# Kernel tuning notes

Hardware: AMD Instinct MI355X
Metric: run time of the kernel (lower is better)

## Reference

```python
import jax, jax.numpy as jnp
import numpy as np

D_MODEL = 768
N_HEADS = 12
D_FF = 3072
EPS = 1e-6


def setup_inputs() -> dict:
    key = jax.random.key(0)
    ks = jax.random.split(key, 9)
    s = 0.02
    return {
        "x": jax.random.normal(ks[0], (2, 4096, D_MODEL), dtype=jnp.float32),
        "wq": jax.random.normal(ks[1], (D_MODEL, D_MODEL), dtype=jnp.float32) * s,
        "wk": jax.random.normal(ks[2], (D_MODEL, D_MODEL), dtype=jnp.float32) * s,
        "wv": jax.random.normal(ks[3], (D_MODEL, D_MODEL), dtype=jnp.float32) * s,
        "wo": jax.random.normal(ks[4], (D_MODEL, D_MODEL), dtype=jnp.float32) * s,
        "w1": jax.random.normal(ks[5], (D_MODEL, D_FF), dtype=jnp.float32) * s,
        "b1": jnp.zeros((D_FF,), dtype=jnp.float32),
        "w2": jax.random.normal(ks[6], (D_FF, D_MODEL), dtype=jnp.float32) * s,
        "b2": jnp.zeros((D_MODEL,), dtype=jnp.float32),
        "g1": jnp.ones((D_MODEL,), dtype=jnp.float32),
        "g2": jnp.ones((D_MODEL,), dtype=jnp.float32),
    }


def _rmsnorm(x, g):
    rms = jax.lax.rsqrt(jnp.mean(x * x, axis=-1, keepdims=True) + EPS)
    return x * rms * g


def _attn(x, wq, wk, wv, wo):
    B, T, D = x.shape
    H, Dh = N_HEADS, D // N_HEADS
    q = (x @ wq).reshape(B, T, H, Dh).transpose(0, 2, 1, 3)
    k = (x @ wk).reshape(B, T, H, Dh).transpose(0, 2, 1, 3)
    v = (x @ wv).reshape(B, T, H, Dh).transpose(0, 2, 1, 3)
    scores = jnp.einsum("bhqd,bhkd->bhqk", q, k) * (Dh ** -0.5)
    causal = jnp.triu(jnp.ones((T, T), dtype=bool), k=1)
    scores = jnp.where(causal, -jnp.inf, scores)
    attn = jax.nn.softmax(scores, axis=-1)
    out = jnp.einsum("bhqk,bhkd->bhqd", attn, v)
    out = out.transpose(0, 2, 1, 3).reshape(B, T, D)
    return out @ wo


def _ffn(x, w1, b1, w2, b2):
    h = jax.nn.gelu(x @ w1 + b1, approximate=False)
    return h @ w2 + b2


def reference(x, wq, wk, wv, wo, w1, b1, w2, b2, g1, g2):
    x = x + _attn(_rmsnorm(x, g1), wq, wk, wv, wo)
    x = x + _ffn(_rmsnorm(x, g2), w1, b1, w2, b2)
    return x
```

## Files before the change

kernel.cpp:

```cpp
#include <hip/hip_runtime.h>
#include <hip/hip_bf16.h>

typedef __attribute__((ext_vector_type(8))) short bf16x8;
typedef __attribute__((ext_vector_type(4))) short bf16x4;
typedef __attribute__((ext_vector_type(4))) float f32x4;

#define MFMA16(a, b, c) __builtin_amdgcn_mfma_f32_16x16x32_bf16((a), (b), (c), 0, 0, 0)

__device__ __forceinline__ f32x4 mfma_k16(bf16x4 a, bf16x4 b, f32x4 c) {
#if __has_builtin(__builtin_amdgcn_mfma_f32_16x16x16bf16_1k)
  return __builtin_amdgcn_mfma_f32_16x16x16bf16_1k(a, b, c, 0, 0, 0);
#elif __has_builtin(__builtin_amdgcn_mfma_f32_16x16x16_bf16)
  return __builtin_amdgcn_mfma_f32_16x16x16_bf16(a, b, c, 0, 0, 0);
#else
  asm("v_mfma_f32_16x16x16_bf16 %0, %1, %2, %0" : "+v"(c) : "v"(a), "v"(b));
  return c;
#endif
}

__device__ __forceinline__ ushort f2bf(float f) {
  union { __hip_bfloat16 h; ushort u; } cv;
  cv.h = __float2bfloat16(f);
  return cv.u;
}

__device__ __forceinline__ void gload16(const void* g, void* l) {
  __builtin_amdgcn_global_load_lds((const __attribute__((address_space(1))) void*)g,
                                   (__attribute__((address_space(3))) void*)l, 16, 0, 0);
}

__global__ void wtrans_all(const float* __restrict__ wq, const float* __restrict__ wk,
                           const float* __restrict__ wv, const float* __restrict__ wo,
                           const float* __restrict__ w1, const float* __restrict__ w2,
                           ushort* __restrict__ wqT, ushort* __restrict__ wkT,
                           ushort* __restrict__ wvT, ushort* __restrict__ woT,
                           ushort* __restrict__ w1T, ushort* __restrict__ w2T) {
  __shared__ float t[32][33];
  int id = blockIdx.x;
  const float* W;
  ushort* Wt;
  int K, N, nbx;
  if (id < 2304) {
    const int m = id / 576;
    id -= m * 576;
    W = (m == 0) ? wq : (m == 1) ? wk : (m == 2) ? wv : wo;
    Wt = (m == 0) ? wqT : (m == 1) ? wkT : (m == 2) ? wvT : woT;
    K = 768; N = 768; nbx = 24;
  } else if (id < 4608) {
    id -= 2304; W = w1; Wt = w1T; K = 768; N = 3072; nbx = 96;
  } else {
    id -= 4608; W = w2; Wt = w2T; K = 3072; N = 768; nbx = 24;
  }
  const int nb = (id % nbx) * 32, kb = (id / nbx) * 32;
  const int tx = threadIdx.x & 31, ty = threadIdx.x >> 5;
#pragma unroll
  for (int i = 0; i < 4; ++i)
    t[ty + i * 8][tx] = W[(size_t)(kb + ty + i * 8) * N + nb + tx];
  __syncthreads();
#pragma unroll
  for (int i = 0; i < 4; ++i)
    Wt[(size_t)(nb + ty + i * 8) * K + kb + tx] = f2bf(t[tx][ty + i * 8]);
}

__global__ void rmsnorm_kernel(const float* __restrict__ x, const float* __restrict__ g,
                               ushort* __restrict__ out) {
  const int row = blockIdx.x;
  const float* xr = x + (size_t)row * 768;
  const int t = threadIdx.x;
  float v0 = xr[t], v1 = xr[t + 256], v2 = xr[t + 512];
  float ss = v0 * v0 + v1 * v1 + v2 * v2;
#pragma unroll
  for (int off = 1; off < 64; off <<= 1) ss += __shfl_xor(ss, off);
  __shared__ float part[4];
  if ((t & 63) == 0) part[t >> 6] = ss;
  __syncthreads();
  const float tot = part[0] + part[1] + part[2] + part[3];
  const float r = rsqrtf(tot * (1.0f / 768.0f) + 1e-6f);
  ushort* orow = out + (size_t)row * 768;
  orow[t]       = f2bf(v0 * r * g[t]);
  orow[t + 256] = f2bf(v1 * r * g[t + 256]);
  orow[t + 512] = f2bf(v2 * r * g[t + 512]);
}

enum { EPI_BF16 = 0, EPI_VT = 1, EPI_RESID = 2, EPI_BIAS_GELU = 3, EPI_BIAS_RESID = 4 };

template <int EPI>
__global__ __launch_bounds__(256) void gemm_bt(
    const ushort* __restrict__ A, const ushort* __restrict__ Bt, void* __restrict__ Cout,
    const float* __restrict__ bias, const float* __restrict__ resid, int M, int N, int K,
    float scale) {
  __shared__ ushort As[2][128 * 64];
  __shared__ ushort Bs[2][128 * 64];
  const int tid = threadIdx.x;
  const int lane = tid & 63, wid = tid >> 6;
  const int wm = wid >> 1, wn = wid & 1;
  const int l15 = lane & 15, l4 = lane >> 4;
  const int m0 = blockIdx.y * 128, n0 = blockIdx.x * 128;
  const int srow = lane >> 3, sslot = lane & 7;
  const int skel = (sslot ^ srow) << 3;

  f32x4 acc[4][4] = {};

#pragma unroll
  for (int i = 0; i < 4; ++i) {
    const int c = i * 4 + wid;
    const int row = c * 8 + srow;
    gload16(A + (size_t)(m0 + row) * K + skel, (char*)As[0] + c * 1024);
    gload16(Bt + (size_t)(n0 + row) * K + skel, (char*)Bs[0] + c * 1024);
  }

  int cur = 0;
  for (int k0 = 0; k0 < K; k0 += 64) {
    if (k0 + 64 < K) {
      char* dA = (char*)As[cur ^ 1];
      char* dB = (char*)Bs[cur ^ 1];
#pragma unroll
      for (int i = 0; i < 4; ++i) {
        const int c = i * 4 + wid;
        const int row = c * 8 + srow;
        gload16(A + (size_t)(m0 + row) * K + k0 + 64 + skel, dA + c * 1024);
        gload16(Bt + (size_t)(n0 + row) * K + k0 + 64 + skel, dB + c * 1024);
      }
      asm volatile("s_waitcnt vmcnt(8)" ::: "memory");
    } else {
      asm volatile("s_waitcnt vmcnt(0)" ::: "memory");
    }
    __builtin_amdgcn_s_barrier();

    const char* pA = (const char*)As[cur];
    const char* pB = (const char*)Bs[cur];
#pragma unroll
    for (int ks = 0; ks < 2; ++ks) {
      bf16x8 af[4], bfr[4];
#pragma unroll
      for (int mi = 0; mi < 4; ++mi) {
        const int row = wm * 64 + mi * 16 + l15;
        const int slot = (ks * 4 + l4) ^ (row & 7);
        af[mi] = *(const bf16x8*)(pA + row * 128 + slot * 16);
      }
#pragma unroll
      for (int ni = 0; ni < 4; ++ni) {
        const int row = wn * 64 + ni * 16 + l15;
        const int slot = (ks * 4 + l4) ^ (row & 7);
        bfr[ni] = *(const bf16x8*)(pB + row * 128 + slot * 16);
      }
#pragma unroll
      for (int mi = 0; mi < 4; ++mi)
#pragma unroll
        for (int ni = 0; ni < 4; ++ni)
          acc[mi][ni] = MFMA16(af[mi], bfr[ni], acc[mi][ni]);
    }
    asm volatile("" ::: "memory");
    __builtin_amdgcn_s_barrier();
    cur ^= 1;
  }

#pragma unroll
  for (int mi = 0; mi < 4; ++mi) {
#pragma unroll
    for (int ni = 0; ni < 4; ++ni) {
      const int gm = m0 + wm * 64 + mi * 16 + l4 * 4;
      const int gn = n0 + wn * 64 + ni * 16 + l15;
      f32x4 v = acc[mi][ni];
#pragma unroll
      for (int r = 0; r < 4; ++r) {
        const size_t idx = (size_t)(gm + r) * N + gn;
        const float f = v[r];
        if constexpr (EPI == EPI_BF16) {
          ((ushort*)Cout)[idx] = f2bf(f * scale);
        } else if constexpr (EPI == EPI_RESID) {
          ((float*)Cout)[idx] = f + resid[idx];
        } else if constexpr (EPI == EPI_BIAS_GELU) {
          const float u = f + bias[gn];
          const float gl = 0.5f * u * (1.0f + erff(u * 0.70710678118654752f));
          ((ushort*)Cout)[idx] = f2bf(gl);
        } else if constexpr (EPI == EPI_BIAS_RESID) {
          ((float*)Cout)[idx] = f + bias[gn] + resid[idx];
        }
      }
    }
  }
}

__global__ __launch_bounds__(256) void gemm_qkv(
    const ushort* __restrict__ A, const ushort* __restrict__ Bt,
    ushort* __restrict__ qout, ushort* __restrict__ kout, ushort* __restrict__ vtout,
    int M, int K, float qscale) {
  __shared__ ushort As[2][128 * 64];
  __shared__ ushort Bs[2][128 * 64];
  const int tid = threadIdx.x;
  const int lane = tid & 63, wid = tid >> 6;
  const int wm = wid >> 1, wn = wid & 1;
  const int l15 = lane & 15, l4 = lane >> 4;
  const int m0 = blockIdx.y * 128, n0 = blockIdx.x * 128;
  const int srow = lane >> 3, sslot = lane & 7;
  const int skel = (sslot ^ srow) << 3;

  f32x4 acc[4][4] = {};

#pragma unroll
  for (int i = 0; i < 4; ++i) {
    const int c = i * 4 + wid;
    const int row = c * 8 + srow;
    gload16(A + (size_t)(m0 + row) * K + skel, (char*)As[0] + c * 1024);
    gload16(Bt + (size_t)(n0 + row) * K + skel, (char*)Bs[0] + c * 1024);
  }

  int cur = 0;
  for (int k0 = 0; k0 < K; k0 += 64) {
    if (k0 + 64 < K) {
      char* dA = (char*)As[cur ^ 1];
      char* dB = (char*)Bs[cur ^ 1];
#pragma unroll
      for (int i = 0; i < 4; ++i) {
        const int c = i * 4 + wid;
        const int row = c * 8 + srow;
        gload16(A + (size_t)(m0 + row) * K + k0 + 64 + skel, dA + c * 1024);
        gload16(Bt + (size_t)(n0 + row) * K + k0 + 64 + skel, dB + c * 1024);
      }
      asm volatile("s_waitcnt vmcnt(8)" ::: "memory");
    } else {
      asm volatile("s_waitcnt vmcnt(0)" ::: "memory");
    }
    __builtin_amdgcn_s_barrier();

    const char* pA = (const char*)As[cur];
    const char* pB = (const char*)Bs[cur];
#pragma unroll
    for (int ks = 0; ks < 2; ++ks) {
      bf16x8 af[4], bfr[4];
#pragma unroll
      for (int mi = 0; mi < 4; ++mi) {
        const int row = wm * 64 + mi * 16 + l15;
        const int slot = (ks * 4 + l4) ^ (row & 7);
        af[mi] = *(const bf16x8*)(pA + row * 128 + slot * 16);
      }
#pragma unroll
      for (int ni = 0; ni < 4; ++ni) {
        const int row = wn * 64 + ni * 16 + l15;
        const int slot = (ks * 4 + l4) ^ (row & 7);
        bfr[ni] = *(const bf16x8*)(pB + row * 128 + slot * 16);
      }
#pragma unroll
      for (int mi = 0; mi < 4; ++mi)
#pragma unroll
        for (int ni = 0; ni < 4; ++ni)
          acc[mi][ni] = MFMA16(af[mi], bfr[ni], acc[mi][ni]);
    }
    asm volatile("" ::: "memory");
    __builtin_amdgcn_s_barrier();
    cur ^= 1;
  }

  const int seg = n0 / 768;
#pragma unroll
  for (int mi = 0; mi < 4; ++mi) {
#pragma unroll
    for (int ni = 0; ni < 4; ++ni) {
      const int gm = m0 + wm * 64 + mi * 16 + l4 * 4;
      const int gn = n0 + wn * 64 + ni * 16 + l15;
      const int col = gn - seg * 768;
      f32x4 v = acc[mi][ni];
      if (seg == 0) {
#pragma unroll
        for (int r = 0; r < 4; ++r)
          qout[(size_t)(gm + r) * 768 + col] = f2bf(v[r] * qscale);
      } else if (seg == 1) {
#pragma unroll
        for (int r = 0; r < 4; ++r)
          kout[(size_t)(gm + r) * 768 + col] = f2bf(v[r]);
      } else {
        const int b = gm >> 12, tt = gm & 4095;
        const int h = col >> 6, dh = col & 63;
        ushort4 pk;
        pk.x = f2bf(v[0]); pk.y = f2bf(v[1]); pk.z = f2bf(v[2]); pk.w = f2bf(v[3]);
        *(ushort4*)(vtout + (((size_t)(b * 12 + h) * 64 + dh) * 4096 + tt)) = pk;
      }
    }
  }
}

__global__ __launch_bounds__(256, 5) void flash_attn_kernel(
    const ushort* __restrict__ Q, const ushort* __restrict__ Kb,
    const ushort* __restrict__ Vt, ushort* __restrict__ O) {
  __shared__ ushort Ks[2][64 * 64];
  __shared__ ushort Vts[2][64 * 64];
  const int tid = threadIdx.x, lane = tid & 63, wid = tid >> 6;
  const int l15 = lane & 15, l4 = lane >> 4;
  const int l7 = l15 & 7;
  const int bid = (int)blockIdx.x;
  const int idx = (bid & 7) * 192 + (bid >> 3);
  const int bh = idx >> 6, b = bh / 12, h = bh % 12;
  const int qb = 63 - (idx & 63);
  const int qbase = qb * 64;
  const int q0 = qbase + wid * 16;

  bf16x8 qf0, qf1;
  {
    const ushort* qp = Q + ((size_t)(b * 4096 + q0 + l15) * 768 + h * 64 + l4 * 8);
    qf0 = *(const bf16x8*)qp;
    qf1 = *(const bf16x8*)(qp + 32);
  }
  f32x4 oo[4] = {};
  float dsum = 0.f;

  const int srow_l = lane >> 3;
  const int sco = ((lane & 7) ^ srow_l) << 3;
  const ushort* Kbase = Kb + (size_t)b * 4096 * 768 + h * 64;
  const ushort* Vbase = Vt + (size_t)bh * 64 * 4096;
  const int c0 = wid, c1 = 4 + wid;
  const ushort* kp0 = Kbase + (size_t)(c0 * 8 + srow_l) * 768 + sco;
  const ushort* kp1 = Kbase + (size_t)(c1 * 8 + srow_l) * 768 + sco;
  const ushort* vp0 = Vbase + (size_t)(c0 * 8 + srow_l) * 4096 + sco;
  const ushort* vp1 = Vbase + (size_t)(c1 * 8 + srow_l) * 4096 + sco;
  const int nt = qb + 1;

  const int koff0 = l15 * 128 + ((l4 ^ l7) << 4);
  const int koff1 = l15 * 128 + (((4 + l4) ^ l7) << 4);
  const int vbase_off = l15 * 128 + ((l4 & 1) << 3);
  const int t2b = l4 >> 1;

  gload16(kp0, (char*)Ks + c0 * 1024);
  gload16(kp1, (char*)Ks + c1 * 1024);
  gload16(vp0, (char*)Vts + c0 * 1024);
  gload16(vp1, (char*)Vts + c1 * 1024);

  int cur = 0;
  for (int kt = 0; kt < nt; ++kt) {
    const int k0 = kt << 6;
    if (kt + 1 < nt) {
      kp0 += 64 * 768; kp1 += 64 * 768;
      vp0 += 64; vp1 += 64;
      const int nb = (cur ^ 1) * 8192;
      gload16(kp0, (char*)Ks + nb + c0 * 1024);
      gload16(kp1, (char*)Ks + nb + c1 * 1024);
      gload16(vp0, (char*)Vts + nb + c0 * 1024);
      gload16(vp1, (char*)Vts + nb + c1 * 1024);
      asm volatile("s_waitcnt vmcnt(4)" ::: "memory");
    } else {
      asm volatile("s_waitcnt vmcnt(0)" ::: "memory");
    }
    __builtin_amdgcn_s_barrier();

    const int nf = (q0 + 16 - k0) >> 4;
    const int nct = nf < 4 ? nf : 4;
    const bool has_diag = (nf <= 4);
    const char* Kc = (const char*)Ks + cur * 8192;
    const char* Vc = (const char*)Vts + cur * 8192;

    __builtin_amdgcn_s_setprio(1);
#pragma unroll
    for (int ct = 0; ct < 4; ++ct) {
      if (ct < nct) {
        f32x4 s = {0.f, 0.f, 0.f, 0.f};
        const bf16x8 kf0 = *(const bf16x8*)(Kc + ct * 2048 + koff0);
        const bf16x8 kf1 = *(const bf16x8*)(Kc + ct * 2048 + koff1);
        s = MFMA16(kf0, qf0, s);
        s = MFMA16(kf1, qf1, s);
        if (has_diag && ct == nct - 1) {
#pragma unroll
          for (int r = 0; r < 4; ++r)
            if (l4 * 4 + r > l15) s[r] = -30.f;
        }
        const float p0 = __builtin_amdgcn_exp2f(s[0]);
        const float p1 = __builtin_amdgcn_exp2f(s[1]);
        const float p2 = __builtin_amdgcn_exp2f(s[2]);
        const float p3 = __builtin_amdgcn_exp2f(s[3]);
        dsum += (p0 + p1) + (p2 + p3);
        union { bf16x4 v; ushort u[4]; } pk;
        pk.u[0] = f2bf(p0); pk.u[1] = f2bf(p1);
        pk.u[2] = f2bf(p2); pk.u[3] = f2bf(p3);
        const int xo = ((2 * ct + t2b) ^ l7) << 4;
#pragma unroll
        for (int dt = 0; dt < 4; ++dt) {
          const bf16x4 vf = *(const bf16x4*)(Vc + dt * 2048 + vbase_off + xo);
          oo[dt] = mfma_k16(pk.v, vf, oo[dt]);
        }
      }
    }
    __builtin_amdgcn_s_setprio(0);
    asm volatile("" ::: "memory");
    __builtin_amdgcn_s_barrier();
    cur ^= 1;
  }

  dsum += __shfl_xor(dsum, 16);
  dsum += __shfl_xor(dsum, 32);
  ushort* op = O + ((size_t)(b * 4096 + q0 + l4 * 4) * 768 + h * 64);
#pragma unroll
  for (int r = 0; r < 4; ++r) {
    const float inv = 1.0f / __shfl(dsum, l4 * 4 + r);
#pragma unroll
    for (int dt = 0; dt < 4; ++dt)
      op[(size_t)r * 768 + dt * 16 + l15] = f2bf(oo[dt][r] * inv);
  }
}

extern "C" void kernel_launch(void* const* d_in, const int* in_sizes, int n_in,
                              void* d_out, int out_size, void* d_ws, size_t ws_size,
                              hipStream_t stream) {
  const float* x  = (const float*)d_in[0];
  const float* wq = (const float*)d_in[1];
  const float* wk = (const float*)d_in[2];
  const float* wv = (const float*)d_in[3];
  const float* wo = (const float*)d_in[4];
  const float* w1 = (const float*)d_in[5];
  const float* b1 = (const float*)d_in[6];
  const float* w2 = (const float*)d_in[7];
  const float* b2 = (const float*)d_in[8];
  const float* g1 = (const float*)d_in[9];
  const float* g2 = (const float*)d_in[10];
  float* out = (float*)d_out;

  char* p = (char*)d_ws;
  ushort* wqT = (ushort*)p; p += (size_t)768 * 768 * 2;
  ushort* wkT = (ushort*)p; p += (size_t)768 * 768 * 2;
  ushort* wvT = (ushort*)p; p += (size_t)768 * 768 * 2;
  ushort* woT = (ushort*)p; p += (size_t)768 * 768 * 2;
  ushort* w1T = (ushort*)p; p += (size_t)3072 * 768 * 2;
  ushort* w2T = (ushort*)p; p += (size_t)768 * 3072 * 2;
  ushort* xn  = (ushort*)p; p += (size_t)8192 * 768 * 2;
  ushort* qb  = (ushort*)p; p += (size_t)8192 * 768 * 2;
  ushort* kb  = (ushort*)p; p += (size_t)8192 * 768 * 2;
  ushort* vtb = (ushort*)p; p += (size_t)8192 * 768 * 2;
  ushort* attn = (ushort*)p; p += (size_t)8192 * 768 * 2;
  float* x2 = (float*)p; p += (size_t)8192 * 768 * 4;
  ushort* hf = qb;

  const float qscale = 0.125f * 1.44269504088896340736f;

  dim3 blk(256);
  wtrans_all<<<dim3(6912), blk, 0, stream>>>(wq, wk, wv, wo, w1, w2,
                                             wqT, wkT, wvT, woT, w1T, w2T);

  rmsnorm_kernel<<<8192, blk, 0, stream>>>(x, g1, xn);

  gemm_qkv<<<dim3(18, 64), blk, 0, stream>>>(xn, wqT, qb, kb, vtb, 8192, 768, qscale);

  flash_attn_kernel<<<dim3(1536), blk, 0, stream>>>(qb, kb, vtb, attn);

  gemm_bt<EPI_RESID><<<dim3(6, 64), blk, 0, stream>>>(attn, woT, x2, nullptr, x, 8192, 768, 768, 1.0f);

  rmsnorm_kernel<<<8192, blk, 0, stream>>>(x2, g2, xn);

  gemm_bt<EPI_BIAS_GELU><<<dim3(24, 64), blk, 0, stream>>>(xn, w1T, hf, b1, nullptr, 8192, 3072, 768, 1.0f);
  gemm_bt<EPI_BIAS_RESID><<<dim3(6, 64), blk, 0, stream>>>(hf, w2T, out, b2, x2, 8192, 768, 3072, 1.0f);
}
```

Before: 326.9 us.

## Split causal flash attention over KV halves and merge partials; vectorize rmsnorm

Each query block's KV range is split into two halves handled by separate blocks. This doubles the attention grid and shortens the longest per-block work, reducing tail imbalance from the causal mask. The halves write unnormalized bf16 partial outputs and row sums, which a new merge kernel adds together and normalizes; the partials reuse the x2 buffer before it is written. RMSNorm now uses float4 loads and ushort4 stores with 192 threads. The cost is an extra kernel pass over the partial outputs, duplicated Q loads, and extra rounding from storing unnormalized partials in bf16.

After: 328.4 us. About the same (+0.4%).

```diff
diff --git a/kernel.cpp b/kernel.cpp
--- a/kernel.cpp
+++ b/kernel.cpp
@@ -22,6 +22,12 @@
   union { __hip_bfloat16 h; ushort u; } cv;
   cv.h = __float2bfloat16(f);
   return cv.u;
+}
+
+__device__ __forceinline__ float bf2f(ushort u) {
+  union { float f; unsigned int i; } c;
+  c.i = ((unsigned int)u) << 16;
+  return c.f;
 }
 
 __device__ __forceinline__ void gload16(const void* g, void* l) {
@@ -64,22 +70,23 @@
 
 __global__ void rmsnorm_kernel(const float* __restrict__ x, const float* __restrict__ g,
                                ushort* __restrict__ out) {
-  const int row = blockIdx.x;
-  const float* xr = x + (size_t)row * 768;
-  const int t = threadIdx.x;
-  float v0 = xr[t], v1 = xr[t + 256], v2 = xr[t + 512];
-  float ss = v0 * v0 + v1 * v1 + v2 * v2;
+  const int row = blockIdx.x, t = threadIdx.x;
+  const float4 v = *(const float4*)(x + (size_t)row * 768 + 4 * t);
+  float ss = v.x * v.x + v.y * v.y + v.z * v.z + v.w * v.w;
 #pragma unroll
   for (int off = 1; off < 64; off <<= 1) ss += __shfl_xor(ss, off);
-  __shared__ float part[4];
+  __shared__ float part[3];
   if ((t & 63) == 0) part[t >> 6] = ss;
   __syncthreads();
-  const float tot = part[0] + part[1] + part[2] + part[3];
+  const float tot = part[0] + part[1] + part[2];
   const float r = rsqrtf(tot * (1.0f / 768.0f) + 1e-6f);
-  ushort* orow = out + (size_t)row * 768;
-  orow[t]       = f2bf(v0 * r * g[t]);
-  orow[t + 256] = f2bf(v1 * r * g[t + 256]);
-  orow[t + 512] = f2bf(v2 * r * g[t + 512]);
+  const float4 gg = *(const float4*)(g + 4 * t);
+  ushort4 o;
+  o.x = f2bf(v.x * r * gg.x);
+  o.y = f2bf(v.y * r * gg.y);
+  o.z = f2bf(v.z * r * gg.z);
+  o.w = f2bf(v.w * r * gg.w);
+  *(ushort4*)(out + (size_t)row * 768 + 4 * t) = o;
 }
 
 enum { EPI_BF16 = 0, EPI_VT = 1, EPI_RESID = 2, EPI_BIAS_GELU = 3, EPI_BIAS_RESID = 4 };
@@ -282,18 +289,24 @@
 
 __global__ __launch_bounds__(256, 5) void flash_attn_kernel(
     const ushort* __restrict__ Q, const ushort* __restrict__ Kb,
-    const ushort* __restrict__ Vt, ushort* __restrict__ O) {
+    const ushort* __restrict__ Vt, ushort* __restrict__ Opart,
+    float* __restrict__ dsb) {
   __shared__ ushort Ks[2][64 * 64];
   __shared__ ushort Vts[2][64 * 64];
   const int tid = threadIdx.x, lane = tid & 63, wid = tid >> 6;
   const int l15 = lane & 15, l4 = lane >> 4;
   const int l7 = l15 & 7;
   const int bid = (int)blockIdx.x;
-  const int idx = (bid & 7) * 192 + (bid >> 3);
-  const int bh = idx >> 6, b = bh / 12, h = bh % 12;
-  const int qb = 63 - (idx & 63);
+  const int idx = (bid & 7) * 384 + (bid >> 3);
+  const int pair = idx >> 1, half = idx & 1;
+  const int bh = pair >> 6, b = bh / 12, h = bh % 12;
+  const int qb = 63 - (pair & 63);
   const int qbase = qb * 64;
   const int q0 = qbase + wid * 16;
+  const int nt = qb + 1;
+  const int h0 = nt >> 1;
+  const int kt0 = half ? h0 : 0;
+  const int kt1 = half ? nt : h0;
 
   bf16x8 qf0, qf1;
   {
@@ -309,26 +322,27 @@
   const ushort* Kbase = Kb + (size_t)b * 4096 * 768 + h * 64;
   const ushort* Vbase = Vt + (size_t)bh * 64 * 4096;
   const int c0 = wid, c1 = 4 + wid;
-  const ushort* kp0 = Kbase + (size_t)(c0 * 8 + srow_l) * 768 + sco;
-  const ushort* kp1 = Kbase + (size_t)(c1 * 8 + srow_l) * 768 + sco;
-  const ushort* vp0 = Vbase + (size_t)(c0 * 8 + srow_l) * 4096 + sco;
-  const ushort* vp1 = Vbase + (size_t)(c1 * 8 + srow_l) * 4096 + sco;
-  const int nt = qb + 1;
+  const ushort* kp0 = Kbase + (size_t)(kt0 * 64 + c0 * 8 + srow_l) * 768 + sco;
+  const ushort* kp1 = Kbase + (size_t)(kt0 * 64 + c1 * 8 + srow_l) * 768 + sco;
+  const ushort* vp0 = Vbase + (size_t)(c0 * 8 + srow_l) * 4096 + kt0 * 64 + sco;
+  const ushort* vp1 = Vbase + (size_t)(c1 * 8 + srow_l) * 4096 + kt0 * 64 + sco;
 
   const int koff0 = l15 * 128 + ((l4 ^ l7) << 4);
   const int koff1 = l15 * 128 + (((4 + l4) ^ l7) << 4);
   const int vbase_off = l15 * 128 + ((l4 & 1) << 3);
   const int t2b = l4 >> 1;
 
-  gload16(kp0, (char*)Ks + c0 * 1024);
-  gload16(kp1, (char*)Ks + c1 * 1024);
-  gload16(vp0, (char*)Vts + c0 * 1024);
-  gload16(vp1, (char*)Vts + c1 * 1024);
+  if (kt0 < kt1) {
+    gload16(kp0, (char*)Ks + c0 * 1024);
+    gload16(kp1, (char*)Ks + c1 * 1024);
+    gload16(vp0, (char*)Vts + c0 * 1024);
+    gload16(vp1, (char*)Vts + c1 * 1024);
+  }
 
   int cur = 0;
-  for (int kt = 0; kt < nt; ++kt) {
+  for (int kt = kt0; kt < kt1; ++kt) {
     const int k0 = kt << 6;
-    if (kt + 1 < nt) {
+    if (kt + 1 < kt1) {
       kp0 += 64 * 768; kp1 += 64 * 768;
       vp0 += 64; vp1 += 64;
       const int nb = (cur ^ 1) * 8192;
@@ -386,14 +400,38 @@
 
   dsum += __shfl_xor(dsum, 16);
   dsum += __shfl_xor(dsum, 32);
-  ushort* op = O + ((size_t)(b * 4096 + q0 + l4 * 4) * 768 + h * 64);
+  if (l4 == 0)
+    dsb[((half * 24 + b * 12 + h) << 12) + q0 + l15] = dsum;
+  ushort* op = Opart + ((size_t)(half * 8192 + b * 4096 + q0 + l4 * 4)) * 768 + h * 64;
 #pragma unroll
   for (int r = 0; r < 4; ++r) {
-    const float inv = 1.0f / __shfl(dsum, l4 * 4 + r);
 #pragma unroll
     for (int dt = 0; dt < 4; ++dt)
-      op[(size_t)r * 768 + dt * 16 + l15] = f2bf(oo[dt][r] * inv);
-  }
+      op[(size_t)r * 768 + dt * 16 + l15] = f2bf(oo[dt][r]);
+  }
+}
+
+__global__ void attn_merge(const ushort* __restrict__ P, const float* __restrict__ ds,
+                           ushort* __restrict__ attn) {
+  const int row = blockIdx.x, t = threadIdx.x;
+  const int b = row >> 12, tr = row & 4095;
+  __shared__ float inv[12];
+  if (t < 12) {
+    const float d0 = ds[((b * 12 + t) << 12) + tr];
+    const float d1 = ds[((24 + b * 12 + t) << 12) + tr];
+    inv[t] = 1.0f / (d0 + d1);
+  }
+  __syncthreads();
+  const size_t o0 = (size_t)row * 768 + 4 * t;
+  const ushort4 a = *(const ushort4*)(P + o0);
+  const ushort4 c = *(const ushort4*)(P + (size_t)8192 * 768 + o0);
+  const float iv = inv[t >> 4];
+  ushort4 o;
+  o.x = f2bf((bf2f(a.x) + bf2f(c.x)) * iv);
+  o.y = f2bf((bf2f(a.y) + bf2f(c.y)) * iv);
+  o.z = f2bf((bf2f(a.z) + bf2f(c.z)) * iv);
+  o.w = f2bf((bf2f(a.w) + bf2f(c.w)) * iv);
+  *(ushort4*)(attn + o0) = o;
 }
 
 extern "C" void kernel_launch(void* const* d_in, const int* in_sizes, int n_in,
@@ -425,7 +463,9 @@
   ushort* vtb = (ushort*)p; p += (size_t)8192 * 768 * 2;
   ushort* attn = (ushort*)p; p += (size_t)8192 * 768 * 2;
   float* x2 = (float*)p; p += (size_t)8192 * 768 * 4;
+  float* dsb = (float*)p; p += (size_t)2 * 24 * 4096 * 4;
   ushort* hf = qb;
+  ushort* Opart = (ushort*)x2;
 
   const float qscale = 0.125f * 1.44269504088896340736f;
 
@@ -433,15 +473,17 @@
   wtrans_all<<<dim3(6912), blk, 0, stream>>>(wq, wk, wv, wo, w1, w2,
                                              wqT, wkT, wvT, woT, w1T, w2T);
 
-  rmsnorm_kernel<<<8192, blk, 0, stream>>>(x, g1, xn);
+  rmsnorm_kernel<<<8192, dim3(192), 0, stream>>>(x, g1, xn);
 
   gemm_qkv<<<dim3(18, 64), blk, 0, stream>>>(xn, wqT, qb, kb, vtb, 8192, 768, qscale);
 
-  flash_attn_kernel<<<dim3(1536), blk, 0, stream>>>(qb, kb, vtb, attn);
+  flash_attn_kernel<<<dim3(3072), blk, 0, stream>>>(qb, kb, vtb, Opart, dsb);
+
+  attn_merge<<<dim3(8192), dim3(192), 0, stream>>>(Opart, dsb, attn);
 
   gemm_bt<EPI_RESID><<<dim3(6, 64), blk, 0, stream>>>(attn, woT, x2, nullptr, x, 8192, 768, 768, 1.0f);
 
-  rmsnorm_kernel<<<8192, blk, 0, stream>>>(x2, g2, xn);
+  rmsnorm_kernel<<<8192, dim3(192), 0, stream>>>(x2, g2, xn);
 
   gemm_bt<EPI_BIAS_GELU><<<dim3(24, 64), blk, 0, stream>>>(xn, w1T, hf, b1, nullptr, 8192, 3072, 768, 1.0f);
   gemm_bt<EPI_BIAS_RESID><<<dim3(6, 64), blk, 0, stream>>>(hf, w2T, out, b2, x2, 8192, 768, 3072, 1.0f);
```
